# Kernel optimization log

Hardware: AMD Instinct MI355X
Metric: run time of the kernel (lower is better)

## Reference

```python
import jax, jax.numpy as jnp
import numpy as np

B, T, U, D = 2, 512, 48, 512
H, K = 1024, 128  # hidden_channels, num_classes; fc1 in = 2*D = 1024


def setup_inputs() -> dict:
    key = jax.random.key(0)
    ks = jax.random.split(key, 9)
    s = 0.02
    return {
        "img_feature": jax.random.normal(ks[0], (B, T, D), jnp.float32),
        "label_feature": jax.random.normal(ks[1], (B, U, D), jnp.float32),
        "masks": jnp.ones((B, 1, T), jnp.float32),
        "W1": jax.random.normal(ks[2], (H, 2 * D), jnp.float32) * s,
        "b1": jnp.zeros((H,), jnp.float32),
        "W2": jax.random.normal(ks[3], (K, H), jnp.float32) * s,
        "b2": jnp.zeros((K,), jnp.float32),
        "conv_w": jax.random.normal(ks[4], (K, D), jnp.float32) * s,
        "conv_b": jnp.zeros((K,), jnp.float32),
    }


def reference(img_feature, label_feature, masks, W1, b1, W2, b2, conv_w, conv_b):
    # pointwise Conv1d over img features: (B,T,D) -> (B,K,T), masked
    img_seg_score = (jnp.einsum('btd,kd->bkt', img_feature, conv_w)
                     + conv_b[None, :, None]) * masks
    # fc1(cat(label, img)) == label @ Wl^T + img @ Wi^T + b1 (broadcast add),
    # avoiding the O(B*U*T*2D) repeat+cat intermediate.
    d = label_feature.shape[-1]
    Wl, Wi = W1[:, :d], W1[:, d:]
    lab = jnp.einsum('bud,hd->buh', label_feature, Wl)  # (B,U,H)
    img = jnp.einsum('btd,hd->bth', img_feature, Wi)    # (B,T,H)
    h = jnp.tanh(lab[:, :, None, :] + img[:, None, :, :] + b1)  # (B,U,T,H)
    joint = jnp.einsum('buth,kh->butk', h, W2) + b2
    joint_score = jax.nn.log_softmax(joint, axis=-1)
    return (img_seg_score, joint_score)
```

## Files before the change

kernel.cpp:

```cpp
#include <hip/hip_runtime.h>
#include <math.h>

#define BB 2
#define TT 512
#define UU 48
#define DD 512
#define HH 1024
#define KK 128

typedef _Float16 f16x8 __attribute__((ext_vector_type(8)));
typedef __fp16 fp16x2_t __attribute__((ext_vector_type(2)));
typedef float floatx4 __attribute__((ext_vector_type(4)));

__device__ __forceinline__ f16x8 tanh8(f16x8 x) {
    f16x8 o;
#pragma unroll
    for (int i = 0; i < 8; i += 2) {
        float s0 = (float)x[i];
        float s1 = (float)x[i + 1];
        float e0 = __expf(s0 + s0);
        float e1 = __expf(s1 + s1);
        float r0 = __builtin_amdgcn_rcpf(e0 + 1.0f);
        float r1 = __builtin_amdgcn_rcpf(e1 + 1.0f);
        fp16x2_t p = __builtin_amdgcn_cvt_pkrtz(fmaf(-2.0f, r0, 1.0f),
                                                fmaf(-2.0f, r1, 1.0f));
        o[i] = (_Float16)p[0];
        o[i + 1] = (_Float16)p[1];
    }
    return o;
}

__global__ __launch_bounds__(256) void mid_kernel4(
    const float* __restrict__ img, const float* __restrict__ labf,
    const float* __restrict__ W1, const float* __restrict__ W2,
    const float* __restrict__ conv_w,
    const float* __restrict__ b1, const float* __restrict__ conv_b,
    const float* __restrict__ masks,
    _Float16* __restrict__ imgHf, _Float16* __restrict__ labHf,
    _Float16* __restrict__ W2s, float* __restrict__ seg_out) {
    int bid = blockIdx.x, tid = threadIdx.x;
    if (bid >= 312) {
        int base = (bid - 312) * 256 + tid;
#pragma unroll
        for (int i = 0; i < 32; ++i) {
            int o = base + i * 4096;
            int hg = o >> 10, kk2 = (o >> 3) & 127, hl = o & 7;
            W2s[o] = (_Float16)W2[(size_t)kk2 * HH + hg * 8 + hl];
        }
        return;
    }
    __shared__ __align__(16) _Float16 a_s[32][72];
    __shared__ __align__(16) _Float16 w_s[8192];
    const float* Arow;
    const float* Wbase;
    int r0, n0b, wstride, region;
    if (bid < 256) {
        region = 0; Arow = img; Wbase = W1 + 512; wstride = 1024;
        r0 = (bid & 31) * 32; n0b = (bid >> 5) * 128;
    } else if (bid < 280) {
        region = 1; Arow = labf; Wbase = W1; wstride = 1024;
        int i = bid - 256; r0 = (i % 3) * 32; n0b = (i / 3) * 128;
    } else {
        region = 2; Arow = img; Wbase = conv_w; wstride = 512;
        r0 = (bid - 280) * 32; n0b = 0;
    }
    int lane = tid & 63, wv = tid >> 6;
    int m0 = (wv & 1) * 16, n0w = (wv >> 1) * 64;
    int q = lane >> 4, r = lane & 15;
    int arow = tid >> 3, acol = (tid & 7) * 8;
    int wn = tid >> 3, wk = tid & 7;
    const float* aptr = &Arow[(size_t)(r0 + arow) * DD + acol];
    floatx4 acc[4] = {};
    float4 pa0, pa1, pw[4][2];
    pa0 = *(const float4*)aptr;
    pa1 = *(const float4*)(aptr + 4);
#pragma unroll
    for (int i2 = 0; i2 < 4; ++i2) {
        const float* wp_ = &Wbase[(size_t)(n0b + i2 * 32 + wn) * wstride + wk * 8];
        pw[i2][0] = *(const float4*)wp_;
        pw[i2][1] = *(const float4*)(wp_ + 4);
    }
    for (int c = 0; c < 8; ++c) {
        {
            f16x8 av;
            av[0] = (_Float16)pa0.x; av[1] = (_Float16)pa0.y;
            av[2] = (_Float16)pa0.z; av[3] = (_Float16)pa0.w;
            av[4] = (_Float16)pa1.x; av[5] = (_Float16)pa1.y;
            av[6] = (_Float16)pa1.z; av[7] = (_Float16)pa1.w;
            *(f16x8*)&a_s[arow][acol] = av;
#pragma unroll
            for (int i2 = 0; i2 < 4; ++i2) {
                f16x8 wvv;
                wvv[0] = (_Float16)pw[i2][0].x; wvv[1] = (_Float16)pw[i2][0].y;
                wvv[2] = (_Float16)pw[i2][0].z; wvv[3] = (_Float16)pw[i2][0].w;
                wvv[4] = (_Float16)pw[i2][1].x; wvv[5] = (_Float16)pw[i2][1].y;
                wvv[6] = (_Float16)pw[i2][1].z; wvv[7] = (_Float16)pw[i2][1].w;
                *(f16x8*)&w_s[((size_t)wk * 128 + i2 * 32 + wn) * 8] = wvv;
            }
        }
        __syncthreads();
        if (c < 7) {
            int cb = (c + 1) * 64;
            pa0 = *(const float4*)(aptr + cb);
            pa1 = *(const float4*)(aptr + cb + 4);
#pragma unroll
            for (int i2 = 0; i2 < 4; ++i2) {
                const float* wp_ =
                    &Wbase[(size_t)(n0b + i2 * 32 + wn) * wstride + cb + wk * 8];
                pw[i2][0] = *(const float4*)wp_;
                pw[i2][1] = *(const float4*)(wp_ + 4);
            }
        }
#pragma unroll
        for (int kt = 0; kt < 2; ++kt) {
            f16x8 af = *(const f16x8*)&a_s[m0 + r][kt * 32 + q * 8];
#pragma unroll
            for (int nt = 0; nt < 4; ++nt) {
                f16x8 bfv = *(const f16x8*)
                    &w_s[((kt * 4 + q) * 128 + n0w + nt * 16 + r) * 8];
                acc[nt] = __builtin_amdgcn_mfma_f32_16x16x32_f16(
                    af, bfv, acc[nt], 0, 0, 0);
            }
        }
        __syncthreads();
    }
    if (region == 0) {
#pragma unroll
        for (int nt = 0; nt < 4; ++nt) {
            int n = n0b + n0w + nt * 16 + r;
#pragma unroll
            for (int rr = 0; rr < 4; ++rr)
                imgHf[(size_t)(r0 + m0 + 4 * q + rr) * HH + n] =
                    (_Float16)acc[nt][rr];
        }
    } else if (region == 1) {
#pragma unroll
        for (int nt = 0; nt < 4; ++nt) {
            int n = n0b + n0w + nt * 16 + r;
            float bv = b1[n];
#pragma unroll
            for (int rr = 0; rr < 4; ++rr)
                labHf[(size_t)(r0 + m0 + 4 * q + rr) * HH + n] =
                    (_Float16)(acc[nt][rr] + bv);
        }
    } else {
#pragma unroll
        for (int nt = 0; nt < 4; ++nt) {
            int k = n0w + nt * 16 + r;
            float bv = conv_b[k];
#pragma unroll
            for (int rr = 0; rr < 4; ++rr) {
                int row = r0 + m0 + 4 * q + rr;
                int b = row >> 9, t = row & 511;
                seg_out[((size_t)b * KK + k) * TT + t] =
                    (acc[nt][rr] + bv) * masks[row];
            }
        }
    }
}

__global__ __launch_bounds__(256) void joint_kernel6(
    const _Float16* __restrict__ imgHf,
    const _Float16* __restrict__ labHf,
    const _Float16* __restrict__ W2s,
    const float* __restrict__ b2,
    float* __restrict__ out) {
    __shared__ __align__(16) _Float16 w_s[2][8192];
    int tid = threadIdx.x, bid = blockIdx.x;
    int t0 = (bid & 7) * 64;
    int rest = bid >> 3;
    int u = rest % UU, b = rest / UU;
    int lane = tid & 63, wv = tid >> 6;
    int q = lane >> 4, r = lane & 15;
    const _Float16* imgrow = imgHf + ((size_t)b * TT + t0 + wv * 16 + r) * HH;
    const _Float16* labrow = labHf + (size_t)(b * UU + u) * HH;
    int c0 = q * 8, c1 = 32 + q * 8;
    int ws_off = tid * 8;
    floatx4 acc[8] = {};
    f16x8 ivA = *(const f16x8*)&imgrow[c0];
    f16x8 ivB = *(const f16x8*)&imgrow[c1];
    f16x8 lvA = *(const f16x8*)&labrow[c0];
    f16x8 lvB = *(const f16x8*)&labrow[c1];
    {
        const _Float16* wsrc = W2s;
#pragma unroll
        for (int i2 = 0; i2 < 4; ++i2)
            *(f16x8*)&w_s[0][i2 * 2048 + ws_off] =
                *(const f16x8*)&wsrc[i2 * 2048 + ws_off];
    }
    __syncthreads();
#pragma unroll 2
    for (int c = 0; c < 16; ++c) {
        int buf = c & 1;
        f16x8 nivA, nivB, nlvA, nlvB, nw0, nw1, nw2, nw3;
        if (c < 15) {
            int cb = (c + 1) * 64;
            nivA = *(const f16x8*)&imgrow[cb + c0];
            nivB = *(const f16x8*)&imgrow[cb + c1];
            nlvA = *(const f16x8*)&labrow[cb + c0];
            nlvB = *(const f16x8*)&labrow[cb + c1];
            const _Float16* wsrc = W2s + (size_t)(c + 1) * 8192;
            nw0 = *(const f16x8*)&wsrc[0 * 2048 + ws_off];
            nw1 = *(const f16x8*)&wsrc[1 * 2048 + ws_off];
            nw2 = *(const f16x8*)&wsrc[2 * 2048 + ws_off];
            nw3 = *(const f16x8*)&wsrc[3 * 2048 + ws_off];
        }
        f16x8 a0 = tanh8(ivA + lvA);
        f16x8 a1 = tanh8(ivB + lvB);
#pragma unroll
        for (int nt = 0; nt < 8; ++nt) {
            f16x8 bf0 = *(const f16x8*)&w_s[buf][((0 + q) * 128 + nt * 16 + r) * 8];
            acc[nt] = __builtin_amdgcn_mfma_f32_16x16x32_f16(
                a0, bf0, acc[nt], 0, 0, 0);
        }
#pragma unroll
        for (int nt = 0; nt < 8; ++nt) {
            f16x8 bf1 = *(const f16x8*)&w_s[buf][((4 + q) * 128 + nt * 16 + r) * 8];
            acc[nt] = __builtin_amdgcn_mfma_f32_16x16x32_f16(
                a1, bf1, acc[nt], 0, 0, 0);
        }
        if (c < 15) {
            *(f16x8*)&w_s[buf ^ 1][0 * 2048 + ws_off] = nw0;
            *(f16x8*)&w_s[buf ^ 1][1 * 2048 + ws_off] = nw1;
            *(f16x8*)&w_s[buf ^ 1][2 * 2048 + ws_off] = nw2;
            *(f16x8*)&w_s[buf ^ 1][3 * 2048 + ws_off] = nw3;
            ivA = nivA; ivB = nivB; lvA = nlvA; lvB = nlvB;
        }
        __syncthreads();
    }
    float b2v[8];
#pragma unroll
    for (int nt = 0; nt < 8; ++nt) b2v[nt] = b2[nt * 16 + r];
    float* orow = out + (((size_t)b * UU + u) * TT + t0 + wv * 16) * KK;
#pragma unroll
    for (int rr = 0; rr < 4; ++rr) {
        float v[8];
        float mx = -INFINITY;
#pragma unroll
        for (int nt = 0; nt < 8; ++nt) {
            v[nt] = acc[nt][rr] + b2v[nt];
            mx = fmaxf(mx, v[nt]);
        }
        mx = fmaxf(mx, __shfl_xor(mx, 1, 16));
        mx = fmaxf(mx, __shfl_xor(mx, 2, 16));
        mx = fmaxf(mx, __shfl_xor(mx, 4, 16));
        mx = fmaxf(mx, __shfl_xor(mx, 8, 16));
        float s = 0.f;
#pragma unroll
        for (int nt = 0; nt < 8; ++nt) s += __expf(v[nt] - mx);
        s += __shfl_xor(s, 1, 16);
        s += __shfl_xor(s, 2, 16);
        s += __shfl_xor(s, 4, 16);
        s += __shfl_xor(s, 8, 16);
        float lse = mx + __logf(s);
        int row = 4 * q + rr;
#pragma unroll
        for (int nt = 0; nt < 8; ++nt)
            orow[(size_t)row * KK + nt * 16 + r] = v[nt] - lse;
    }
}

extern "C" void kernel_launch(void* const* d_in, const int* in_sizes, int n_in,
                              void* d_out, int out_size, void* d_ws, size_t ws_size,
                              hipStream_t stream) {
    const float* img    = (const float*)d_in[0];
    const float* labf   = (const float*)d_in[1];
    const float* masks  = (const float*)d_in[2];
    const float* W1     = (const float*)d_in[3];
    const float* b1     = (const float*)d_in[4];
    const float* W2     = (const float*)d_in[5];
    const float* b2     = (const float*)d_in[6];
    const float* conv_w = (const float*)d_in[7];
    const float* conv_b = (const float*)d_in[8];
    float* out = (float*)d_out;

    _Float16* base  = (_Float16*)d_ws;
    _Float16* imgHf = base;
    _Float16* labHf = imgHf + 1024 * 1024;
    _Float16* W2s   = labHf + 96 * 1024;

    mid_kernel4<<<328, 256, 0, stream>>>(img, labf, W1, W2, conv_w,
                                         b1, conv_b, masks,
                                         imgHf, labHf, W2s, out);
    joint_kernel6<<<768, 256, 0, stream>>>(imgHf, labHf, W2s, b2,
                                           out + (size_t)BB * KK * TT);
}
```

Before: 124.7 us.

## Retile both kernels, fold tanh scale into fp16 projections, use exp2

The joint kernel now gives each wave two 16-row tiles over a flattened (b,u,t) row index, so every W2 fragment read from LDS feeds two MFMAs. It runs 192-thread blocks with an occupancy hint and 512 blocks instead of 768. The first kernel halves its N tile to 64, doubling the block count, and remaps region-0 blocks with an XCD-aware interleave. The 2/ln2 factor for tanh is folded into the stored fp16 projections, so tanh can use a raw exp2. The scaled fp16 values carry slightly more rounding error, and the wider accumulators raise register pressure.

```diff
diff --git a/kernel.cpp b/kernel.cpp
--- a/kernel.cpp
+++ b/kernel.cpp
@@ -12,14 +12,12 @@
 typedef __fp16 fp16x2_t __attribute__((ext_vector_type(2)));
 typedef float floatx4 __attribute__((ext_vector_type(4)));
 
-__device__ __forceinline__ f16x8 tanh8(f16x8 x) {
+__device__ __forceinline__ f16x8 tanh8z(f16x8 z) {
     f16x8 o;
 #pragma unroll
     for (int i = 0; i < 8; i += 2) {
-        float s0 = (float)x[i];
-        float s1 = (float)x[i + 1];
-        float e0 = __expf(s0 + s0);
-        float e1 = __expf(s1 + s1);
+        float e0 = __builtin_amdgcn_exp2f((float)z[i]);
+        float e1 = __builtin_amdgcn_exp2f((float)z[i + 1]);
         float r0 = __builtin_amdgcn_rcpf(e0 + 1.0f);
         float r1 = __builtin_amdgcn_rcpf(e1 + 1.0f);
         fp16x2_t p = __builtin_amdgcn_cvt_pkrtz(fmaf(-2.0f, r0, 1.0f),
@@ -30,7 +28,7 @@
     return o;
 }
 
-__global__ __launch_bounds__(256) void mid_kernel4(
+__global__ __launch_bounds__(256) void mid_kernel5(
     const float* __restrict__ img, const float* __restrict__ labf,
     const float* __restrict__ W1, const float* __restrict__ W2,
     const float* __restrict__ conv_w,
@@ -39,8 +37,8 @@
     _Float16* __restrict__ imgHf, _Float16* __restrict__ labHf,
     _Float16* __restrict__ W2s, float* __restrict__ seg_out) {
     int bid = blockIdx.x, tid = threadIdx.x;
-    if (bid >= 312) {
-        int base = (bid - 312) * 256 + tid;
+    if (bid >= 624) {
+        int base = (bid - 624) * 256 + tid;
 #pragma unroll
         for (int i = 0; i < 32; ++i) {
             int o = base + i * 4096;
@@ -50,103 +48,99 @@
         return;
     }
     __shared__ __align__(16) _Float16 a_s[32][72];
-    __shared__ __align__(16) _Float16 w_s[8192];
+    __shared__ __align__(16) _Float16 w_s[4096];
     const float* Arow;
     const float* Wbase;
     int r0, n0b, wstride, region;
-    if (bid < 256) {
-        region = 0; Arow = img; Wbase = W1 + 512; wstride = 1024;
-        r0 = (bid & 31) * 32; n0b = (bid >> 5) * 128;
-    } else if (bid < 280) {
-        region = 1; Arow = labf; Wbase = W1; wstride = 1024;
-        int i = bid - 256; r0 = (i % 3) * 32; n0b = (i / 3) * 128;
+    if (bid < 512) {
+        region = 0; Arow = img; Wbase = W1 + 512; wstride = 2 * DD;
+        int xcd = bid & 7, j = bid >> 3;
+        r0 = (j & 31) * 32; n0b = (xcd * 2 + (j >> 5)) * 64;
+    } else if (bid < 560) {
+        region = 1; Arow = labf; Wbase = W1; wstride = 2 * DD;
+        int i = bid - 512; r0 = (i % 3) * 32; n0b = (i / 3) * 64;
     } else {
-        region = 2; Arow = img; Wbase = conv_w; wstride = 512;
-        r0 = (bid - 280) * 32; n0b = 0;
+        region = 2; Arow = img; Wbase = conv_w; wstride = DD;
+        int i = bid - 560; r0 = (i >> 1) * 32; n0b = (i & 1) * 64;
     }
     int lane = tid & 63, wv = tid >> 6;
-    int m0 = (wv & 1) * 16, n0w = (wv >> 1) * 64;
+    int m0 = (wv & 1) * 16, n0w = (wv >> 1) * 32;
     int q = lane >> 4, r = lane & 15;
     int arow = tid >> 3, acol = (tid & 7) * 8;
-    int wn = tid >> 3, wk = tid & 7;
+    int wn = tid >> 2, wk0 = (tid & 3) * 16;
     const float* aptr = &Arow[(size_t)(r0 + arow) * DD + acol];
-    floatx4 acc[4] = {};
-    float4 pa0, pa1, pw[4][2];
+    const float* wptr = &Wbase[(size_t)(n0b + wn) * wstride + wk0];
+    floatx4 acc[2] = {};
+    float4 pa0, pa1, pw[4];
     pa0 = *(const float4*)aptr;
     pa1 = *(const float4*)(aptr + 4);
 #pragma unroll
-    for (int i2 = 0; i2 < 4; ++i2) {
-        const float* wp_ = &Wbase[(size_t)(n0b + i2 * 32 + wn) * wstride + wk * 8];
-        pw[i2][0] = *(const float4*)wp_;
-        pw[i2][1] = *(const float4*)(wp_ + 4);
-    }
+    for (int i2 = 0; i2 < 4; ++i2) pw[i2] = *(const float4*)(wptr + i2 * 4);
     for (int c = 0; c < 8; ++c) {
-        {
-            f16x8 av;
-            av[0] = (_Float16)pa0.x; av[1] = (_Float16)pa0.y;
-            av[2] = (_Float16)pa0.z; av[3] = (_Float16)pa0.w;
-            av[4] = (_Float16)pa1.x; av[5] = (_Float16)pa1.y;
-            av[6] = (_Float16)pa1.z; av[7] = (_Float16)pa1.w;
-            *(f16x8*)&a_s[arow][acol] = av;
-#pragma unroll
-            for (int i2 = 0; i2 < 4; ++i2) {
-                f16x8 wvv;
-                wvv[0] = (_Float16)pw[i2][0].x; wvv[1] = (_Float16)pw[i2][0].y;
-                wvv[2] = (_Float16)pw[i2][0].z; wvv[3] = (_Float16)pw[i2][0].w;
-                wvv[4] = (_Float16)pw[i2][1].x; wvv[5] = (_Float16)pw[i2][1].y;
-                wvv[6] = (_Float16)pw[i2][1].z; wvv[7] = (_Float16)pw[i2][1].w;
-                *(f16x8*)&w_s[((size_t)wk * 128 + i2 * 32 + wn) * 8] = wvv;
-            }
-        }
+        f16x8 av;
+        av[0] = (_Float16)pa0.x; av[1] = (_Float16)pa0.y;
+        av[2] = (_Float16)pa0.z; av[3] = (_Float16)pa0.w;
+        av[4] = (_Float16)pa1.x; av[5] = (_Float16)pa1.y;
+        av[6] = (_Float16)pa1.z; av[7] = (_Float16)pa1.w;
+        *(f16x8*)&a_s[arow][acol] = av;
+        f16x8 w0, w1;
+        w0[0] = (_Float16)pw[0].x; w0[1] = (_Float16)pw[0].y;
+        w0[2] = (_Float16)pw[0].z; w0[3] = (_Float16)pw[0].w;
+        w0[4] = (_Float16)pw[1].x; w0[5] = (_Float16)pw[1].y;
+        w0[6] = (_Float16)pw[1].z; w0[7] = (_Float16)pw[1].w;
+        w1[0] = (_Float16)pw[2].x; w1[1] = (_Float16)pw[2].y;
+        w1[2] = (_Float16)pw[2].z; w1[3] = (_Float16)pw[2].w;
+        w1[4] = (_Float16)pw[3].x; w1[5] = (_Float16)pw[3].y;
+        w1[6] = (_Float16)pw[3].z; w1[7] = (_Float16)pw[3].w;
+        int kg = wk0 >> 3;
+        *(f16x8*)&w_s[((kg + 0) * 64 + wn) * 8] = w0;
+        *(f16x8*)&w_s[((kg + 1) * 64 + wn) * 8] = w1;
         __syncthreads();
         if (c < 7) {
             int cb = (c + 1) * 64;
             pa0 = *(const float4*)(aptr + cb);
             pa1 = *(const float4*)(aptr + cb + 4);
 #pragma unroll
-            for (int i2 = 0; i2 < 4; ++i2) {
-                const float* wp_ =
-                    &Wbase[(size_t)(n0b + i2 * 32 + wn) * wstride + cb + wk * 8];
-                pw[i2][0] = *(const float4*)wp_;
-                pw[i2][1] = *(const float4*)(wp_ + 4);
-            }
+            for (int i2 = 0; i2 < 4; ++i2)
+                pw[i2] = *(const float4*)(wptr + cb + i2 * 4);
         }
 #pragma unroll
         for (int kt = 0; kt < 2; ++kt) {
             f16x8 af = *(const f16x8*)&a_s[m0 + r][kt * 32 + q * 8];
 #pragma unroll
-            for (int nt = 0; nt < 4; ++nt) {
-                f16x8 bfv = *(const f16x8*)
-                    &w_s[((kt * 4 + q) * 128 + n0w + nt * 16 + r) * 8];
+            for (int nt = 0; nt < 2; ++nt) {
+                f16x8 bf = *(const f16x8*)
+                    &w_s[((kt * 4 + q) * 64 + n0w + nt * 16 + r) * 8];
                 acc[nt] = __builtin_amdgcn_mfma_f32_16x16x32_f16(
-                    af, bfv, acc[nt], 0, 0, 0);
+                    af, bf, acc[nt], 0, 0, 0);
             }
         }
         __syncthreads();
     }
+    const float SC = 2.8853900817779268f;
     if (region == 0) {
 #pragma unroll
-        for (int nt = 0; nt < 4; ++nt) {
+        for (int nt = 0; nt < 2; ++nt) {
             int n = n0b + n0w + nt * 16 + r;
 #pragma unroll
             for (int rr = 0; rr < 4; ++rr)
                 imgHf[(size_t)(r0 + m0 + 4 * q + rr) * HH + n] =
-                    (_Float16)acc[nt][rr];
+                    (_Float16)(acc[nt][rr] * SC);
         }
     } else if (region == 1) {
 #pragma unroll
-        for (int nt = 0; nt < 4; ++nt) {
+        for (int nt = 0; nt < 2; ++nt) {
             int n = n0b + n0w + nt * 16 + r;
             float bv = b1[n];
 #pragma unroll
             for (int rr = 0; rr < 4; ++rr)
                 labHf[(size_t)(r0 + m0 + 4 * q + rr) * HH + n] =
-                    (_Float16)(acc[nt][rr] + bv);
+                    (_Float16)((acc[nt][rr] + bv) * SC);
         }
     } else {
 #pragma unroll
-        for (int nt = 0; nt < 4; ++nt) {
-            int k = n0w + nt * 16 + r;
+        for (int nt = 0; nt < 2; ++nt) {
+            int k = n0b + n0w + nt * 16 + r;
             float bv = conv_b[k];
 #pragma unroll
             for (int rr = 0; rr < 4; ++rr) {
@@ -159,7 +153,7 @@
     }
 }
 
-__global__ __launch_bounds__(256) void joint_kernel6(
+__global__ __launch_bounds__(192, 2) void joint_kernel7(
     const _Float16* __restrict__ imgHf,
     const _Float16* __restrict__ labHf,
     const _Float16* __restrict__ W2s,
@@ -167,96 +161,115 @@
     float* __restrict__ out) {
     __shared__ __align__(16) _Float16 w_s[2][8192];
     int tid = threadIdx.x, bid = blockIdx.x;
-    int t0 = (bid & 7) * 64;
-    int rest = bid >> 3;
-    int u = rest % UU, b = rest / UU;
     int lane = tid & 63, wv = tid >> 6;
     int q = lane >> 4, r = lane & 15;
-    const _Float16* imgrow = imgHf + ((size_t)b * TT + t0 + wv * 16 + r) * HH;
-    const _Float16* labrow = labHf + (size_t)(b * UU + u) * HH;
+    int g0 = bid * 96 + wv * 32;
+    int gr0 = g0 + r, gr1 = g0 + 16 + r;
+    int bu0 = gr0 >> 9, t0 = gr0 & 511;
+    int bu1 = gr1 >> 9, t1 = gr1 & 511;
+    const _Float16* ir0 = imgHf + (size_t)(((bu0 >= UU) ? TT : 0) + t0) * HH;
+    const _Float16* ir1 = imgHf + (size_t)(((bu1 >= UU) ? TT : 0) + t1) * HH;
+    const _Float16* lr0 = labHf + (size_t)bu0 * HH;
+    const _Float16* lr1 = labHf + (size_t)bu1 * HH;
     int c0 = q * 8, c1 = 32 + q * 8;
-    int ws_off = tid * 8;
-    floatx4 acc[8] = {};
-    f16x8 ivA = *(const f16x8*)&imgrow[c0];
-    f16x8 ivB = *(const f16x8*)&imgrow[c1];
-    f16x8 lvA = *(const f16x8*)&labrow[c0];
-    f16x8 lvB = *(const f16x8*)&labrow[c1];
-    {
-        const _Float16* wsrc = W2s;
-#pragma unroll
-        for (int i2 = 0; i2 < 4; ++i2)
-            *(f16x8*)&w_s[0][i2 * 2048 + ws_off] =
-                *(const f16x8*)&wsrc[i2 * 2048 + ws_off];
-    }
+    floatx4 acc0[8] = {}, acc1[8] = {};
+#pragma unroll
+    for (int j = 0; j < 5; ++j)
+        *(f16x8*)&w_s[0][(tid + j * 192) * 8] =
+            *(const f16x8*)&W2s[(tid + j * 192) * 8];
+    if (tid < 64)
+        *(f16x8*)&w_s[0][(tid + 960) * 8] = *(const f16x8*)&W2s[(tid + 960) * 8];
+    f16x8 i0A = *(const f16x8*)&ir0[c0], i0B = *(const f16x8*)&ir0[c1];
+    f16x8 i1A = *(const f16x8*)&ir1[c0], i1B = *(const f16x8*)&ir1[c1];
+    f16x8 l0A = *(const f16x8*)&lr0[c0], l0B = *(const f16x8*)&lr0[c1];
+    f16x8 l1A = *(const f16x8*)&lr1[c0], l1B = *(const f16x8*)&lr1[c1];
     __syncthreads();
-#pragma unroll 2
     for (int c = 0; c < 16; ++c) {
-        int buf = c & 1;
-        f16x8 nivA, nivB, nlvA, nlvB, nw0, nw1, nw2, nw3;
+        _Float16* wb = w_s[c & 1];
+        f16x8 ni0A, ni0B, ni1A, ni1B, nl0A, nl0B, nl1A, nl1B;
+        f16x8 nw0, nw1, nw2, nw3, nw4, nw5;
         if (c < 15) {
             int cb = (c + 1) * 64;
-            nivA = *(const f16x8*)&imgrow[cb + c0];
-            nivB = *(const f16x8*)&imgrow[cb + c1];
-            nlvA = *(const f16x8*)&labrow[cb + c0];
-            nlvB = *(const f16x8*)&labrow[cb + c1];
+            ni0A = *(const f16x8*)&ir0[cb + c0];
+            ni0B = *(const f16x8*)&ir0[cb + c1];
+            ni1A = *(const f16x8*)&ir1[cb + c0];
+            ni1B = *(const f16x8*)&ir1[cb + c1];
+            nl0A = *(const f16x8*)&lr0[cb + c0];
+            nl0B = *(const f16x8*)&lr0[cb + c1];
+            nl1A = *(const f16x8*)&lr1[cb + c0];
+            nl1B = *(const f16x8*)&lr1[cb + c1];
             const _Float16* wsrc = W2s + (size_t)(c + 1) * 8192;
-            nw0 = *(const f16x8*)&wsrc[0 * 2048 + ws_off];
-            nw1 = *(const f16x8*)&wsrc[1 * 2048 + ws_off];
-            nw2 = *(const f16x8*)&wsrc[2 * 2048 + ws_off];
-            nw3 = *(const f16x8*)&wsrc[3 * 2048 + ws_off];
-        }
-        f16x8 a0 = tanh8(ivA + lvA);
-        f16x8 a1 = tanh8(ivB + lvB);
+            nw0 = *(const f16x8*)&wsrc[(tid + 0 * 192) * 8];
+            nw1 = *(const f16x8*)&wsrc[(tid + 1 * 192) * 8];
+            nw2 = *(const f16x8*)&wsrc[(tid + 2 * 192) * 8];
+            nw3 = *(const f16x8*)&wsrc[(tid + 3 * 192) * 8];
+            nw4 = *(const f16x8*)&wsrc[(tid + 4 * 192) * 8];
+            if (tid < 64) nw5 = *(const f16x8*)&wsrc[(tid + 960) * 8];
+        }
+        f16x8 a0A = tanh8z(i0A + l0A);
+        f16x8 a1A = tanh8z(i1A + l1A);
 #pragma unroll
         for (int nt = 0; nt < 8; ++nt) {
-            f16x8 bf0 = *(const f16x8*)&w_s[buf][((0 + q) * 128 + nt * 16 + r) * 8];
-            acc[nt] = __builtin_amdgcn_mfma_f32_16x16x32_f16(
-                a0, bf0, acc[nt], 0, 0, 0);
-        }
+            f16x8 bf = *(const f16x8*)&wb[(q * 128 + nt * 16 + r) * 8];
+            acc0[nt] = __builtin_amdgcn_mfma_f32_16x16x32_f16(
+                a0A, bf, acc0[nt], 0, 0, 0);
+            acc1[nt] = __builtin_amdgcn_mfma_f32_16x16x32_f16(
+                a1A, bf, acc1[nt], 0, 0, 0);
+        }
+        f16x8 a0B = tanh8z(i0B + l0B);
+        f16x8 a1B = tanh8z(i1B + l1B);
 #pragma unroll
         for (int nt = 0; nt < 8; ++nt) {
-            f16x8 bf1 = *(const f16x8*)&w_s[buf][((4 + q) * 128 + nt * 16 + r) * 8];
-            acc[nt] = __builtin_amdgcn_mfma_f32_16x16x32_f16(
-                a1, bf1, acc[nt], 0, 0, 0);
+            f16x8 bf = *(const f16x8*)&wb[((4 + q) * 128 + nt * 16 + r) * 8];
+            acc0[nt] = __builtin_amdgcn_mfma_f32_16x16x32_f16(
+                a0B, bf, acc0[nt], 0, 0, 0);
+            acc1[nt] = __builtin_amdgcn_mfma_f32_16x16x32_f16(
+                a1B, bf, acc1[nt], 0, 0, 0);
         }
         if (c < 15) {
-            *(f16x8*)&w_s[buf ^ 1][0 * 2048 + ws_off] = nw0;
-            *(f16x8*)&w_s[buf ^ 1][1 * 2048 + ws_off] = nw1;
-            *(f16x8*)&w_s[buf ^ 1][2 * 2048 + ws_off] = nw2;
-            *(f16x8*)&w_s[buf ^ 1][3 * 2048 + ws_off] = nw3;
-            ivA = nivA; ivB = nivB; lvA = nlvA; lvB = nlvB;
+            _Float16* wn_ = w_s[(c & 1) ^ 1];
+            *(f16x8*)&wn_[(tid + 0 * 192) * 8] = nw0;
+            *(f16x8*)&wn_[(tid + 1 * 192) * 8] = nw1;
+            *(f16x8*)&wn_[(tid + 2 * 192) * 8] = nw2;
+            *(f16x8*)&wn_[(tid + 3 * 192) * 8] = nw3;
+            *(f16x8*)&wn_[(tid + 4 * 192) * 8] = nw4;
+            if (tid < 64) *(f16x8*)&wn_[(tid + 960) * 8] = nw5;
+            i0A = ni0A; i0B = ni0B; i1A = ni1A; i1B = ni1B;
+            l0A = nl0A; l0B = nl0B; l1A = nl1A; l1B = nl1B;
         }
         __syncthreads();
     }
     float b2v[8];
 #pragma unroll
     for (int nt = 0; nt < 8; ++nt) b2v[nt] = b2[nt * 16 + r];
-    float* orow = out + (((size_t)b * UU + u) * TT + t0 + wv * 16) * KK;
-#pragma unroll
-    for (int rr = 0; rr < 4; ++rr) {
-        float v[8];
-        float mx = -INFINITY;
-#pragma unroll
-        for (int nt = 0; nt < 8; ++nt) {
-            v[nt] = acc[nt][rr] + b2v[nt];
-            mx = fmaxf(mx, v[nt]);
-        }
-        mx = fmaxf(mx, __shfl_xor(mx, 1, 16));
-        mx = fmaxf(mx, __shfl_xor(mx, 2, 16));
-        mx = fmaxf(mx, __shfl_xor(mx, 4, 16));
-        mx = fmaxf(mx, __shfl_xor(mx, 8, 16));
-        float s = 0.f;
-#pragma unroll
-        for (int nt = 0; nt < 8; ++nt) s += __expf(v[nt] - mx);
-        s += __shfl_xor(s, 1, 16);
-        s += __shfl_xor(s, 2, 16);
-        s += __shfl_xor(s, 4, 16);
-        s += __shfl_xor(s, 8, 16);
-        float lse = mx + __logf(s);
-        int row = 4 * q + rr;
-#pragma unroll
-        for (int nt = 0; nt < 8; ++nt)
-            orow[(size_t)row * KK + nt * 16 + r] = v[nt] - lse;
+#pragma unroll
+    for (int mt = 0; mt < 2; ++mt) {
+        float* obase = out + (size_t)(g0 + mt * 16 + 4 * q) * KK;
+#pragma unroll
+        for (int rr = 0; rr < 4; ++rr) {
+            float v[8];
+            float mx = -INFINITY;
+#pragma unroll
+            for (int nt = 0; nt < 8; ++nt) {
+                v[nt] = (mt ? acc1[nt][rr] : acc0[nt][rr]) + b2v[nt];
+                mx = fmaxf(mx, v[nt]);
+            }
+            mx = fmaxf(mx, __shfl_xor(mx, 1, 16));
+            mx = fmaxf(mx, __shfl_xor(mx, 2, 16));
+            mx = fmaxf(mx, __shfl_xor(mx, 4, 16));
+            mx = fmaxf(mx, __shfl_xor(mx, 8, 16));
+            float s = 0.f;
+#pragma unroll
+            for (int nt = 0; nt < 8; ++nt) s += __expf(v[nt] - mx);
+            s += __shfl_xor(s, 1, 16);
+            s += __shfl_xor(s, 2, 16);
+            s += __shfl_xor(s, 4, 16);
+            s += __shfl_xor(s, 8, 16);
+            float lse = mx + __logf(s);
+#pragma unroll
+            for (int nt = 0; nt < 8; ++nt)
+                obase[(size_t)rr * KK + nt * 16 + r] = v[nt] - lse;
+        }
     }
 }
 
@@ -279,9 +292,9 @@
     _Float16* labHf = imgHf + 1024 * 1024;
     _Float16* W2s   = labHf + 96 * 1024;
 
-    mid_kernel4<<<328, 256, 0, stream>>>(img, labf, W1, W2, conv_w,
+    mid_kernel5<<<640, 256, 0, stream>>>(img, labf, W1, W2, conv_w,
                                          b1, conv_b, masks,
                                          imgHf, labHf, W2s, out);
-    joint_kernel6<<<768, 256, 0, stream>>>(imgHf, labHf, W2s, b2,
+    joint_kernel7<<<512, 192, 0, stream>>>(imgHf, labHf, W2s, b2,
                                            out + (size_t)BB * KK * TT);
 }
```

After: 125.9 us. Within noise of the previous version (+1.0%).
